# Kernel optimization log

Measured on AMD Instinct MI355X. Metric: run time of the kernel, lower is better.

Reference implementation:

```python
import jax, jax.numpy as jnp
import numpy as np

N = 10000
E = 320000
D_IN = 256
D_H = 256
D_OUT = 64
NEG_SLOPE = 0.2


def _segment_softmax(scores, seg, num_segments):
    # numerically stable softmax over variable-size neighborhoods
    m = jax.ops.segment_max(scores, seg, num_segments=num_segments)
    e = jnp.exp(scores - m[seg])
    s = jax.ops.segment_sum(e, seg, num_segments=num_segments)
    return e / s[seg]


def _gatv2_conv(x, src, dst, Wl, bl, Wr, br, att, bias):
    # PyG GATv2Conv, heads=1: lin_l on source, lin_r on target
    xl = x @ Wl + bl              # [N, C]
    xr = x @ Wr + br              # [N, C]
    xj = xl[src]                  # [E, C] source messages
    e = jax.nn.leaky_relu(xj + xr[dst], NEG_SLOPE)   # [E, C]
    score = e @ att               # [E]
    alpha = _segment_softmax(score, dst, N)          # [E]
    out = jax.ops.segment_sum(alpha[:, None] * xj, dst, num_segments=N)
    return out + bias


def setup_inputs() -> dict:
    key = jax.random.key(0)
    ks = jax.random.split(key, 16)
    s1 = 1.0 / np.sqrt(D_IN)
    s2 = 1.0 / np.sqrt(D_H)
    x = jax.random.normal(ks[0], (N, D_IN), dtype=jnp.float32)
    edge_index = jax.random.randint(ks[1], (2, E), 0, N, dtype=jnp.int64)
    return {
        "x": x,
        "W1l": jax.random.normal(ks[2], (D_IN, D_H), jnp.float32) * s1,
        "b1l": jnp.zeros((D_H,), jnp.float32),
        "W1r": jax.random.normal(ks[3], (D_IN, D_H), jnp.float32) * s1,
        "b1r": jnp.zeros((D_H,), jnp.float32),
        "att1": jax.random.normal(ks[4], (D_H,), jnp.float32) * s2,
        "bias1": jnp.zeros((D_H,), jnp.float32),
        "W2l": jax.random.normal(ks[5], (D_H, D_H), jnp.float32) * s2,
        "b2l": jnp.zeros((D_H,), jnp.float32),
        "W2r": jax.random.normal(ks[6], (D_H, D_H), jnp.float32) * s2,
        "b2r": jnp.zeros((D_H,), jnp.float32),
        "att2": jax.random.normal(ks[7], (D_H,), jnp.float32) * s2,
        "bias2": jnp.zeros((D_H,), jnp.float32),
        "Wout": jax.random.normal(ks[8], (D_H, D_OUT), jnp.float32) * s2,
        "bout": jnp.zeros((D_OUT,), jnp.float32),
        "edge_index": edge_index,
    }


def reference(x, W1l, b1l, W1r, b1r, att1, bias1,
              W2l, b2l, W2r, b2r, att2, bias2,
              Wout, bout, edge_index):
    # add self loops (PyG GATv2Conv default)
    loops = jnp.arange(N, dtype=edge_index.dtype)
    src = jnp.concatenate([edge_index[0], loops])
    dst = jnp.concatenate([edge_index[1], loops])

    h = _gatv2_conv(x, src, dst, W1l, b1l, W1r, b1r, att1, bias1)
    h = jax.nn.relu(h)            # norm=Identity, dropout inactive (eval)
    h = _gatv2_conv(h, src, dst, W2l, b2l, W2r, b2r, att2, bias2)
    h = jax.nn.relu(h)
    logits = h @ Wout + bout      # [N, D_OUT]
    return jax.nn.log_softmax(logits, axis=1)
```

## Files before the change

### kernel.cpp

```cpp
#include <hip/hip_runtime.h>
#include <hip/hip_bf16.h>
#include <math.h>

#define N_NODES 10000
#define N_EDGES 320000
#define TOT_E (N_EDGES + N_NODES)
#define D 256
#define DOUT 64
#define NEG_SLOPE 0.2f
#define MAXDEG 128

typedef __attribute__((ext_vector_type(8))) short bf16x8;
typedef __attribute__((ext_vector_type(4))) float f32x4;
typedef unsigned short ushort_t;

__device__ __forceinline__ unsigned short f2b_rne(float f) {
    unsigned int x = __float_as_uint(f);
    x += 0x7FFFu + ((x >> 16) & 1u);
    return (unsigned short)(x >> 16);
}
__device__ __forceinline__ float b2f(unsigned short h) {
    return __uint_as_float(((unsigned int)h) << 16);
}
__device__ __forceinline__ void bsplit(float v, unsigned short& hi, unsigned short& lo) {
    hi = f2b_rne(v);
    lo = f2b_rne(v - b2f(hi));
}

__device__ __forceinline__ void gload16(const ushort_t* g, ushort_t* l) {
    __builtin_amdgcn_global_load_lds(
        (const __attribute__((address_space(1))) void*)g,
        (__attribute__((address_space(3))) void*)l, 16, 0, 0);
}

__device__ __forceinline__ bool detect_f32(const void* x) {
    const ushort_t* xb = (const ushort_t*)x;
    int lane = threadIdx.x & 63;
    int bad = 0;
    #pragma unroll
    for (int i = 0; i < 4; ++i) {
        float v = b2f(xb[2 * (lane + 64 * i)]);
        bad += !(fabsf(v) < 1e4f) ? 1 : 0;
    }
    #pragma unroll
    for (int o = 32; o > 0; o >>= 1) bad += __shfl_down(bad, o);
    return __shfl(bad, 0) > 8;
}
__device__ __forceinline__ bool detect_i64(const int* e32) {
    int lane = threadIdx.x & 63;
    int nz = (e32[2 * lane + 1] != 0) ? 1 : 0;
    #pragma unroll
    for (int o = 32; o > 0; o >>= 1) nz += __shfl_down(nz, o);
    return __shfl(nz, 0) == 0;
}

__global__ __launch_bounds__(256) void prep_kernel(
        const void* x, ushort_t* xh, ushort_t* xlo,
        const void* W1l, const void* W1r, const void* W2l, const void* W2r, const void* Wo,
        const void* v0, const void* v1, const void* v2, const void* v3,
        const void* v4, const void* v5, const void* v6, const void* v7, const void* v8,
        ushort_t* wt, float* vecf, int* counts) {
    bool f32s = detect_f32(x);
    int bid = blockIdx.x;
    int t = threadIdx.x;
    if (bid < 2500) {
        int i = bid * 1024 + t * 4;
        float v[4];
        if (f32s) {
            float4 f = *(const float4*)((const float*)x + i);
            v[0] = f.x; v[1] = f.y; v[2] = f.z; v[3] = f.w;
        } else {
            union { uint2 q; ushort_t u[4]; } r;
            r.q = *(const uint2*)((const ushort_t*)x + i);
            #pragma unroll
            for (int j = 0; j < 4; ++j) v[j] = b2f(r.u[j]);
        }
        union { uint2 q; ushort_t u[4]; } H, L;
        #pragma unroll
        for (int j = 0; j < 4; ++j) bsplit(v[j], H.u[j], L.u[j]);
        *(uint2*)(xh + i) = H.q;
        *(uint2*)(xlo + i) = L.q;
    } else if (bid < 3588) {
        int b = bid - 2500;
        const void* srcs5[5] = {W1l, W1r, W2l, W2r, Wo};
        int wid, n, ncols;
        if (b < 1024) { wid = b >> 8; n = b & 255; ncols = 256; }
        else          { wid = 4;      n = b - 1024; ncols = 64; }
        ushort_t* dh;
        ushort_t* dl;
        if (wid < 4) { dh = wt + (size_t)wid * 2 * 65536; dl = dh + 65536; }
        else         { dh = wt + (size_t)8 * 65536;       dl = dh + 16384; }
        float v = f32s ? ((const float*)srcs5[wid])[(size_t)t * ncols + n]
                       : b2f(((const ushort_t*)srcs5[wid])[(size_t)t * ncols + n]);
        unsigned short hi, lo;
        bsplit(v, hi, lo);
        dh[(size_t)n * 256 + t] = hi;
        dl[(size_t)n * 256 + t] = lo;
    } else if (bid < 3597) {
        int b = bid - 3588;
        const void* ps[9] = {v0, v1, v2, v3, v4, v5, v6, v7, v8};
        int n = (b == 8) ? DOUT : 256;
        if (t < n) {
            float v = f32s ? ((const float*)ps[b])[t] : b2f(((const ushort_t*)ps[b])[t]);
            vecf[b * 256 + t] = v;
        }
    } else {
        int idx = (bid - 3597) * 256 + t;
        if (idx < N_NODES) counts[idx] = 0;
    }
}

__device__ __forceinline__ int eload(const int* ei, bool is64, int idx) {
    int v = is64 ? ei[2 * (size_t)idx] : ei[idx];
    return ((unsigned)v < (unsigned)N_NODES) ? v : 0;
}

__global__ __launch_bounds__(256) void scatter_kernel(const int* __restrict__ ei,
                                                      int* __restrict__ counts,
                                                      int* __restrict__ srcs_pad) {
    bool is64 = detect_i64(ei);
    int id = blockIdx.x * 256 + threadIdx.x;
    if (id >= TOT_E) return;
    int src, dst;
    if (id < N_EDGES) { src = eload(ei, is64, id); dst = eload(ei, is64, N_EDGES + id); }
    else              { src = dst = id - N_EDGES; }
    int slot = atomicAdd(&counts[dst], 1);
    if (slot < MAXDEG) srcs_pad[dst * MAXDEG + slot] = src;
}

__global__ __launch_bounds__(256, 3) void gemm_mfma_kernel(
        const ushort_t* __restrict__ Ahg, const ushort_t* __restrict__ Alg,
        const ushort_t* __restrict__ Wh0, const ushort_t* __restrict__ Wl0,
        const float* __restrict__ bias0, ushort_t* __restrict__ out0,
        const ushort_t* __restrict__ Wh1, const ushort_t* __restrict__ Wl1,
        const float* __restrict__ bias1, ushort_t* __restrict__ out1) {
    __shared__ __align__(16) ushort_t AhL[2][4096];
    __shared__ __align__(16) ushort_t AlL[2][4096];
    __shared__ __align__(16) ushort_t BhL[2][2048];
    __shared__ __align__(16) ushort_t BlL[2][2048];
    int tid = threadIdx.x;
    int lane = tid & 63, wave = tid >> 6;
    int lin = blockIdx.x + 8 * blockIdx.y;
    int v = (lin & 7) * 79 + (lin >> 3);
    int row0 = (v >> 3) * 128;
    int y = v & 7;
    const ushort_t* Wh; const ushort_t* Wl; const float* bias;
    ushort_t* outp;
    int col0;
    if (y < 4) { Wh = Wh0; Wl = Wl0; bias = bias0; col0 = y * 64; outp = out0; }
    else       { Wh = Wh1; Wl = Wl1; bias = bias1; col0 = (y - 4) * 64; outp = out1; }

    const ushort_t* gp[6];
    ushort_t* lp0[6];
    ushort_t* lp1[6];
    {
        int lane4 = lane >> 2;
        int qsl = (lane & 3) ^ (lane4 & 3);
        #pragma unroll
        for (int j = 0; j < 6; ++j) {
            int q = wave * 6 + j;
            if (q < 8) {
                gp[j] = Ahg + (size_t)(row0 + q * 16 + lane4) * 256 + qsl * 8;
                lp0[j] = &AhL[0][q * 512]; lp1[j] = &AhL[1][q * 512];
            } else if (q < 16) {
                int r = q - 8;
                gp[j] = Alg + (size_t)(row0 + r * 16 + lane4) * 256 + qsl * 8;
                lp0[j] = &AlL[0][r * 512]; lp1[j] = &AlL[1][r * 512];
            } else if (q < 20) {
                int r = q - 16;
                gp[j] = Wh + (size_t)(col0 + r * 16 + lane4) * 256 + qsl * 8;
                lp0[j] = &BhL[0][r * 512]; lp1[j] = &BhL[1][r * 512];
            } else {
                int r = q - 20;
                gp[j] = Wl + (size_t)(col0 + r * 16 + lane4) * 256 + qsl * 8;
                lp0[j] = &BlL[0][r * 512]; lp1[j] = &BlL[1][r * 512];
            }
        }
    }
    int wm = wave >> 1, wn = wave & 1;
    int l15 = lane & 15;
    int slot = (lane >> 4) ^ (lane & 3);

    f32x4 acc[4][2];
    #pragma unroll
    for (int mg = 0; mg < 4; ++mg)
        #pragma unroll
        for (int ng = 0; ng < 2; ++ng) acc[mg][ng] = (f32x4){0.f, 0.f, 0.f, 0.f};

    #pragma unroll
    for (int j = 0; j < 6; ++j) { gload16(gp[j], lp0[j]); gp[j] += 32; }
    __syncthreads();

    #pragma unroll
    for (int s = 0; s < 8; ++s) {
        const int cb = s & 1;
        if (s < 7) {
            #pragma unroll
            for (int j = 0; j < 6; ++j) {
                gload16(gp[j], cb ? lp0[j] : lp1[j]);
                gp[j] += 32;
            }
        }
        bf16x8 ah[4], al[4];
        #pragma unroll
        for (int mg = 0; mg < 4; ++mg) {
            int o = (wm * 64 + mg * 16 + l15) * 32 + slot * 8;
            ah[mg] = *(const bf16x8*)&AhL[cb][o];
            al[mg] = *(const bf16x8*)&AlL[cb][o];
        }
        #pragma unroll
        for (int ng = 0; ng < 2; ++ng) {
            int o = (wn * 32 + ng * 16 + l15) * 32 + slot * 8;
            bf16x8 b_h = *(const bf16x8*)&BhL[cb][o];
            bf16x8 b_l = *(const bf16x8*)&BlL[cb][o];
            #pragma unroll
            for (int mg = 0; mg < 4; ++mg) {
                acc[mg][ng] = __builtin_amdgcn_mfma_f32_16x16x32_bf16(ah[mg], b_l, acc[mg][ng], 0, 0, 0);
                acc[mg][ng] = __builtin_amdgcn_mfma_f32_16x16x32_bf16(al[mg], b_h, acc[mg][ng], 0, 0, 0);
                acc[mg][ng] = __builtin_amdgcn_mfma_f32_16x16x32_bf16(ah[mg], b_h, acc[mg][ng], 0, 0, 0);
            }
        }
        __syncthreads();
    }

    int quad = lane >> 4;
    #pragma unroll
    for (int ng = 0; ng < 2; ++ng) {
        int col = col0 + wn * 32 + ng * 16 + l15;
        float bv = bias[col];
        #pragma unroll
        for (int mg = 0; mg < 4; ++mg) {
            #pragma unroll
            for (int i = 0; i < 4; ++i) {
                int row = row0 + wm * 64 + mg * 16 + quad * 4 + i;
                if (row < N_NODES) {
                    float vv = acc[mg][ng][i] + bv;
                    outp[(size_t)row * D + col] = f2b_rne(vv);
                }
            }
        }
    }
}

__global__ __launch_bounds__(256) void quant_kernel(const ushort_t* __restrict__ xin,
                                                    unsigned char* __restrict__ xq,
                                                    float* __restrict__ xscale) {
    int lane = threadIdx.x & 63;
    int row = blockIdx.x * 4 + (threadIdx.x >> 6);
    if (row >= N_NODES) return;
    union { uint2 q; ushort_t u[4]; } r;
    r.q = *(const uint2*)(xin + (size_t)row * D + lane * 4);
    float v[4];
    float am = 0.f;
    #pragma unroll
    for (int j = 0; j < 4; ++j) {
        v[j] = b2f(r.u[j]);
        if (!isfinite(v[j])) v[j] = 0.f;
        am = fmaxf(am, fabsf(v[j]));
    }
    #pragma unroll
    for (int o = 32; o > 0; o >>= 1) am = fmaxf(am, __shfl_xor(am, o));
    float inv = (am > 0.f) ? 127.f / am : 0.f;
    unsigned int pk = 0;
    #pragma unroll
    for (int j = 0; j < 4; ++j) {
        int qv = (int)rintf(v[j] * inv);
        pk |= ((unsigned int)(qv & 255)) << (8 * j);
    }
    *(unsigned int*)(xq + (size_t)row * D + lane * 4) = pk;
    if (lane == 0) xscale[row] = (am > 0.f) ? am / 127.f : 0.f;
}

__global__ __launch_bounds__(256) void conv_kernel(const unsigned char* __restrict__ xq,
                                                   const float* __restrict__ xscale,
                                                   const ushort_t* __restrict__ xrb,
                                                   const float* __restrict__ att,
                                                   const float* __restrict__ bias,
                                                   const int* __restrict__ counts,
                                                   const int* __restrict__ srcs_pad,
                                                   ushort_t* __restrict__ hh,
                                                   ushort_t* __restrict__ hl) {
    __shared__ float fbuf[8][256];
    __shared__ float sred[8];
    int node = blockIdx.x;
    int t = threadIdx.x;
    int lane = t & 63;
    int hw = t >> 5;
    int seg = t & 31;
    int deg = counts[node];
    if (deg > MAXDEG) deg = MAXDEG;
    if (deg <= 0) {
        float o = fmaxf(bias[t], 0.f);
        unsigned short hi, lo; bsplit(o, hi, lo);
        hh[(size_t)node * D + t] = hi;
        hl[(size_t)node * D + t] = lo;
        return;
    }
    int s0 = srcs_pad[node * MAXDEG + lane];
    int s1 = srcs_pad[node * MAXDEG + 64 + lane];
    float xr8[8], att8[8];
    {
        union { uint4 q; ushort_t u[8]; } rr;
        rr.q = *(const uint4*)(xrb + (size_t)node * D + seg * 8);
        float4 a0 = *(const float4*)(att + seg * 8);
        float4 a1 = *(const float4*)(att + seg * 8 + 4);
        #pragma unroll
        for (int j = 0; j < 8; ++j) xr8[j] = b2f(rr.u[j]);
        att8[0] = a0.x; att8[1] = a0.y; att8[2] = a0.z; att8[3] = a0.w;
        att8[4] = a1.x; att8[5] = a1.y; att8[6] = a1.z; att8[7] = a1.w;
    }
    float acc8[8];
    #pragma unroll
    for (int j = 0; j < 8; ++j) acc8[j] = 0.f;
    float s = 0.f;

    for (int e0 = 0; e0 < deg; e0 += 32) {
        int dlim = deg - e0; if (dlim > 32) dlim = 32;
        int ni = (dlim > hw) ? ((dlim - hw + 7) >> 3) : 0;
        uint2 r[4];
        float se[4];
        #pragma unroll
        for (int i = 0; i < 4; ++i) {
            if (i < ni) {
                int e = e0 + hw + 8 * i;
                int src = __shfl((e < 64) ? s0 : s1, e & 63);
                r[i] = *(const uint2*)(xq + (size_t)src * D + seg * 8);
                se[i] = xscale[src];
            }
        }
        #pragma unroll
        for (int i = 0; i < 4; ++i) {
            if (i < ni) {
                float xf[8];
                #pragma unroll
                for (int j = 0; j < 8; ++j) {
                    unsigned int w32 = (j < 4) ? r[i].x : r[i].y;
                    int iv = ((int)(w32 << (24 - 8 * (j & 3)))) >> 24;
                    xf[j] = (float)iv * se[i];
                }
                float p = 0.f;
                #pragma unroll
                for (int j = 0; j < 8; ++j) {
                    float v = xf[j] + xr8[j];
                    v = fmaxf(v, NEG_SLOPE * v);
                    p = fmaf(v, att8[j], p);
                }
                #pragma unroll
                for (int o = 16; o > 0; o >>= 1) p += __shfl_xor(p, o, 32);
                p = __expf(fminf(fmaxf(p, -80.f), 80.f));
                s += p;
                #pragma unroll
                for (int j = 0; j < 8; ++j) acc8[j] = fmaf(p, xf[j], acc8[j]);
            }
        }
    }
    *(float4*)&fbuf[hw][seg * 8] = (float4){acc8[0], acc8[1], acc8[2], acc8[3]};
    *(float4*)&fbuf[hw][seg * 8 + 4] = (float4){acc8[4], acc8[5], acc8[6], acc8[7]};
    if (seg == 0) sred[hw] = s;
    __syncthreads();
    float tot = 0.f;
    #pragma unroll
    for (int k = 0; k < 8; ++k) tot += fbuf[k][t];
    float stot = sred[0];
    #pragma unroll
    for (int k = 1; k < 8; ++k) stot += sred[k];
    float o = tot / stot + bias[t];
    if (!isfinite(o)) o = 0.f;
    o = fmaxf(o, 0.f);
    unsigned short hi, lo; bsplit(o, hi, lo);
    hh[(size_t)node * D + t] = hi;
    hl[(size_t)node * D + t] = lo;
}

__global__ __launch_bounds__(256) void logits_kernel(
        const ushort_t* __restrict__ Ahg, const ushort_t* __restrict__ Alg,
        const ushort_t* __restrict__ Wh, const ushort_t* __restrict__ Wl,
        const float* __restrict__ bias, float* __restrict__ out) {
    __shared__ bf16x8 Ah[4][64];
    __shared__ bf16x8 Al[4][64];
    __shared__ bf16x8 Bh[4][64];
    __shared__ bf16x8 Bl[4][64];
    __shared__ float Cs[64][65];
    __shared__ float mxs[64], lss[64];
    int tid = threadIdx.x;
    int lane = tid & 63, wave = tid >> 6;
    int row0 = blockIdx.x * 64;
    int sm = tid >> 2, skq = tid & 3;
    int sl = skq * 16 + (sm & 15), sr = sm >> 4;

    f32x4 acc[4];
    #pragma unroll
    for (int c = 0; c < 4; ++c) acc[c] = (f32x4){0.f, 0.f, 0.f, 0.f};

    for (int k0 = 0; k0 < D; k0 += 32) {
        uint4 qah, qal;
        int grow = row0 + sm;
        if (grow < N_NODES) {
            size_t aoff = (size_t)grow * D + k0 + skq * 8;
            qah = *(const uint4*)(Ahg + aoff);
            qal = *(const uint4*)(Alg + aoff);
        } else {
            qah = (uint4){0, 0, 0, 0}; qal = (uint4){0, 0, 0, 0};
        }
        size_t boff = (size_t)sm * 256 + k0 + skq * 8;
        uint4 qbh = *(const uint4*)(Wh + boff);
        uint4 qbl = *(const uint4*)(Wl + boff);
        __syncthreads();
        *(uint4*)&Ah[sr][sl] = qah;
        *(uint4*)&Al[sr][sl] = qal;
        *(uint4*)&Bh[sr][sl] = qbh;
        *(uint4*)&Bl[sr][sl] = qbl;
        __syncthreads();
        bf16x8 a_h = Ah[wave][lane];
        bf16x8 a_l = Al[wave][lane];
        #pragma unroll
        for (int c = 0; c < 4; ++c) {
            bf16x8 b_h = Bh[c][lane];
            bf16x8 b_l = Bl[c][lane];
            acc[c] = __builtin_amdgcn_mfma_f32_16x16x32_bf16(a_h, b_l, acc[c], 0, 0, 0);
            acc[c] = __builtin_amdgcn_mfma_f32_16x16x32_bf16(a_l, b_h, acc[c], 0, 0, 0);
            acc[c] = __builtin_amdgcn_mfma_f32_16x16x32_bf16(a_h, b_h, acc[c], 0, 0, 0);
        }
    }
    int quad = lane >> 4;
    #pragma unroll
    for (int c = 0; c < 4; ++c) {
        int col = c * 16 + (lane & 15);
        float bv = bias[col];
        #pragma unroll
        for (int i = 0; i < 4; ++i) {
            int row = wave * 16 + quad * 4 + i;
            Cs[row][col] = acc[c][i] + bv;
        }
    }
    __syncthreads();
    if (tid < 64) {
        float mx = -INFINITY;
        for (int c2 = 0; c2 < 64; ++c2) {
            float v = Cs[tid][c2];
            if (!isfinite(v)) { v = -1e30f; Cs[tid][c2] = v; }
            mx = fmaxf(mx, v);
        }
        float ssum = 0.f;
        for (int c2 = 0; c2 < 64; ++c2) ssum += expf(Cs[tid][c2] - mx);
        mxs[tid] = mx;
        lss[tid] = logf(ssum);
    }
    __syncthreads();
    for (int idx = tid; idx < 64 * 64; idx += 256) {
        int r = idx >> 6, col = idx & 63;
        int grow = row0 + r;
        if (grow < N_NODES) out[(size_t)grow * DOUT + col] = Cs[r][col] - mxs[r] - lss[r];
    }
}

extern "C" void kernel_launch(void* const* d_in, const int* in_sizes, int n_in,
                              void* d_out, int out_size, void* d_ws, size_t ws_size,
                              hipStream_t stream) {
    const void* x    = d_in[0];
    const void* W1l  = d_in[1];
    const void* b1l  = d_in[2];
    const void* W1r  = d_in[3];
    const void* b1r  = d_in[4];
    const void* att1 = d_in[5];
    const void* bia1 = d_in[6];
    const void* W2l  = d_in[7];
    const void* b2l  = d_in[8];
    const void* W2r  = d_in[9];
    const void* b2r  = d_in[10];
    const void* att2 = d_in[11];
    const void* bia2 = d_in[12];
    const void* Wout = d_in[13];
    const void* bout = d_in[14];
    const int*  ei   = (const int*)d_in[15];

    int* counts   = (int*)d_ws;
    int* srcs_pad = counts + N_NODES;
    ushort_t* wt = (ushort_t*)(srcs_pad + (size_t)N_NODES * MAXDEG);
    ushort_t* W1lH = wt;                ushort_t* W1lL = W1lH + 65536;
    ushort_t* W1rH = W1lL + 65536;      ushort_t* W1rL = W1rH + 65536;
    ushort_t* W2lH = W1rL + 65536;      ushort_t* W2lL = W2lH + 65536;
    ushort_t* W2rH = W2lL + 65536;      ushort_t* W2rL = W2rH + 65536;
    ushort_t* WoH  = W2rL + 65536;      ushort_t* WoL  = WoH + 16384;
    float* vecf = (float*)(WoL + 16384);
    ushort_t* xh  = (ushort_t*)(vecf + 9 * 256);
    ushort_t* xlo = xh + (size_t)N_NODES * D;
    ushort_t* xlb = xlo + (size_t)N_NODES * D;
    ushort_t* xrb = xlb + (size_t)N_NODES * D;
    unsigned char* xq = (unsigned char*)(xrb + (size_t)N_NODES * D);
    float* xscale = (float*)(xq + (size_t)N_NODES * D);
    ushort_t* hh = xh;
    ushort_t* hl = xlo;

    float* b1lf = vecf + 0 * 256;
    float* b1rf = vecf + 1 * 256;
    float* att1f = vecf + 2 * 256;
    float* bia1f = vecf + 3 * 256;
    float* b2lf = vecf + 4 * 256;
    float* b2rf = vecf + 5 * 256;
    float* att2f = vecf + 6 * 256;
    float* bia2f = vecf + 7 * 256;
    float* boutf = vecf + 8 * 256;

    prep_kernel<<<3637, 256, 0, stream>>>(x, xh, xlo,
                                          W1l, W1r, W2l, W2r, Wout,
                                          b1l, b1r, att1, bia1, b2l, b2r, att2, bia2, bout,
                                          wt, vecf, counts);
    scatter_kernel<<<(TOT_E + 255) / 256, 256, 0, stream>>>(ei, counts, srcs_pad);

    gemm_mfma_kernel<<<dim3(8, 79), 256, 0, stream>>>(
        xh, xlo, W1lH, W1lL, b1lf, xlb, W1rH, W1rL, b1rf, xrb);
    quant_kernel<<<(N_NODES + 3) / 4, 256, 0, stream>>>(xlb, xq, xscale);
    conv_kernel<<<N_NODES, 256, 0, stream>>>(xq, xscale, xrb, att1f, bia1f,
                                             counts, srcs_pad, hh, hl);
    gemm_mfma_kernel<<<dim3(8, 79), 256, 0, stream>>>(
        hh, hl, W2lH, W2lL, b2lf, xlb, W2rH, W2rL, b2rf, xrb);
    quant_kernel<<<(N_NODES + 3) / 4, 256, 0, stream>>>(xlb, xq, xscale);
    conv_kernel<<<N_NODES, 256, 0, stream>>>(xq, xscale, xrb, att2f, bia2f,
                                             counts, srcs_pad, hh, hl);
    logits_kernel<<<(N_NODES + 63) / 64, 256, 0, stream>>>(hh, hl, WoH, WoL, boutf, (float*)d_out);
}
```

Baseline: 237.5 us.

## Fold edge scatter into first GEMM launch and gather bf16 messages directly

The edge scatter, which builds the padded neighbor lists, now runs as extra blocks appended to the first GEMM grid, removing a separate launch and letting it overlap with GEMM tiles. The int8 quantization kernels are removed, and the conv kernel gathers bf16 source rows directly. This drops two launches and the quantize pass, but doubles the bytes read per gathered neighbor (16 instead of 8 per segment). It also removes an approximation, since int8 messages reduced accuracy.

```diff
diff --git a/kernel.cpp b/kernel.cpp
--- a/kernel.cpp
+++ b/kernel.cpp
@@ -115,31 +115,34 @@
     return ((unsigned)v < (unsigned)N_NODES) ? v : 0;
 }
 
-__global__ __launch_bounds__(256) void scatter_kernel(const int* __restrict__ ei,
-                                                      int* __restrict__ counts,
-                                                      int* __restrict__ srcs_pad) {
-    bool is64 = detect_i64(ei);
-    int id = blockIdx.x * 256 + threadIdx.x;
-    if (id >= TOT_E) return;
-    int src, dst;
-    if (id < N_EDGES) { src = eload(ei, is64, id); dst = eload(ei, is64, N_EDGES + id); }
-    else              { src = dst = id - N_EDGES; }
-    int slot = atomicAdd(&counts[dst], 1);
-    if (slot < MAXDEG) srcs_pad[dst * MAXDEG + slot] = src;
-}
-
 __global__ __launch_bounds__(256, 3) void gemm_mfma_kernel(
         const ushort_t* __restrict__ Ahg, const ushort_t* __restrict__ Alg,
         const ushort_t* __restrict__ Wh0, const ushort_t* __restrict__ Wl0,
         const float* __restrict__ bias0, ushort_t* __restrict__ out0,
         const ushort_t* __restrict__ Wh1, const ushort_t* __restrict__ Wl1,
-        const float* __restrict__ bias1, ushort_t* __restrict__ out1) {
+        const float* __restrict__ bias1, ushort_t* __restrict__ out1,
+        const int* __restrict__ ei, int* __restrict__ counts,
+        int* __restrict__ srcs_pad) {
     __shared__ __align__(16) ushort_t AhL[2][4096];
     __shared__ __align__(16) ushort_t AlL[2][4096];
     __shared__ __align__(16) ushort_t BhL[2][2048];
     __shared__ __align__(16) ushort_t BlL[2][2048];
     int tid = threadIdx.x;
     int lane = tid & 63, wave = tid >> 6;
+
+    if (blockIdx.y >= 79) {
+        bool is64 = detect_i64(ei);
+        int id = ((blockIdx.y - 79) * 8 + blockIdx.x) * 256 + tid;
+        if (id < TOT_E) {
+            int src, dst;
+            if (id < N_EDGES) { src = eload(ei, is64, id); dst = eload(ei, is64, N_EDGES + id); }
+            else              { src = dst = id - N_EDGES; }
+            int slot = atomicAdd(&counts[dst], 1);
+            if (slot < MAXDEG) srcs_pad[dst * MAXDEG + slot] = src;
+        }
+        return;
+    }
+
     int lin = blockIdx.x + 8 * blockIdx.y;
     int v = (lin & 7) * 79 + (lin >> 3);
     int row0 = (v >> 3) * 128;
@@ -242,37 +245,7 @@
     }
 }
 
-__global__ __launch_bounds__(256) void quant_kernel(const ushort_t* __restrict__ xin,
-                                                    unsigned char* __restrict__ xq,
-                                                    float* __restrict__ xscale) {
-    int lane = threadIdx.x & 63;
-    int row = blockIdx.x * 4 + (threadIdx.x >> 6);
-    if (row >= N_NODES) return;
-    union { uint2 q; ushort_t u[4]; } r;
-    r.q = *(const uint2*)(xin + (size_t)row * D + lane * 4);
-    float v[4];
-    float am = 0.f;
-    #pragma unroll
-    for (int j = 0; j < 4; ++j) {
-        v[j] = b2f(r.u[j]);
-        if (!isfinite(v[j])) v[j] = 0.f;
-        am = fmaxf(am, fabsf(v[j]));
-    }
-    #pragma unroll
-    for (int o = 32; o > 0; o >>= 1) am = fmaxf(am, __shfl_xor(am, o));
-    float inv = (am > 0.f) ? 127.f / am : 0.f;
-    unsigned int pk = 0;
-    #pragma unroll
-    for (int j = 0; j < 4; ++j) {
-        int qv = (int)rintf(v[j] * inv);
-        pk |= ((unsigned int)(qv & 255)) << (8 * j);
-    }
-    *(unsigned int*)(xq + (size_t)row * D + lane * 4) = pk;
-    if (lane == 0) xscale[row] = (am > 0.f) ? am / 127.f : 0.f;
-}
-
-__global__ __launch_bounds__(256) void conv_kernel(const unsigned char* __restrict__ xq,
-                                                   const float* __restrict__ xscale,
+__global__ __launch_bounds__(256) void conv_kernel(const ushort_t* __restrict__ xl,
                                                    const ushort_t* __restrict__ xrb,
                                                    const float* __restrict__ att,
                                                    const float* __restrict__ bias,
@@ -317,15 +290,13 @@
     for (int e0 = 0; e0 < deg; e0 += 32) {
         int dlim = deg - e0; if (dlim > 32) dlim = 32;
         int ni = (dlim > hw) ? ((dlim - hw + 7) >> 3) : 0;
-        uint2 r[4];
-        float se[4];
+        union { uint4 q; ushort_t u[8]; } r[4];
         #pragma unroll
         for (int i = 0; i < 4; ++i) {
             if (i < ni) {
                 int e = e0 + hw + 8 * i;
                 int src = __shfl((e < 64) ? s0 : s1, e & 63);
-                r[i] = *(const uint2*)(xq + (size_t)src * D + seg * 8);
-                se[i] = xscale[src];
+                r[i].q = *(const uint4*)(xl + (size_t)src * D + seg * 8);
             }
         }
         #pragma unroll
@@ -333,11 +304,7 @@
             if (i < ni) {
                 float xf[8];
                 #pragma unroll
-                for (int j = 0; j < 8; ++j) {
-                    unsigned int w32 = (j < 4) ? r[i].x : r[i].y;
-                    int iv = ((int)(w32 << (24 - 8 * (j & 3)))) >> 24;
-                    xf[j] = (float)iv * se[i];
-                }
+                for (int j = 0; j < 8; ++j) xf[j] = b2f(r[i].u[j]);
                 float p = 0.f;
                 #pragma unroll
                 for (int j = 0; j < 8; ++j) {
@@ -487,8 +454,6 @@
     ushort_t* xlo = xh + (size_t)N_NODES * D;
     ushort_t* xlb = xlo + (size_t)N_NODES * D;
     ushort_t* xrb = xlb + (size_t)N_NODES * D;
-    unsigned char* xq = (unsigned char*)(xrb + (size_t)N_NODES * D);
-    float* xscale = (float*)(xq + (size_t)N_NODES * D);
     ushort_t* hh = xh;
     ushort_t* hl = xlo;
 
@@ -506,17 +471,16 @@
                                           W1l, W1r, W2l, W2r, Wout,
                                           b1l, b1r, att1, bia1, b2l, b2r, att2, bia2, bout,
                                           wt, vecf, counts);
-    scatter_kernel<<<(TOT_E + 255) / 256, 256, 0, stream>>>(ei, counts, srcs_pad);
-
-    gemm_mfma_kernel<<<dim3(8, 79), 256, 0, stream>>>(
-        xh, xlo, W1lH, W1lL, b1lf, xlb, W1rH, W1rL, b1rf, xrb);
-    quant_kernel<<<(N_NODES + 3) / 4, 256, 0, stream>>>(xlb, xq, xscale);
-    conv_kernel<<<N_NODES, 256, 0, stream>>>(xq, xscale, xrb, att1f, bia1f,
+
+    gemm_mfma_kernel<<<dim3(8, 79 + 162), 256, 0, stream>>>(
+        xh, xlo, W1lH, W1lL, b1lf, xlb, W1rH, W1rL, b1rf, xrb,
+        ei, counts, srcs_pad);
+    conv_kernel<<<N_NODES, 256, 0, stream>>>(xlb, xrb, att1f, bia1f,
                                              counts, srcs_pad, hh, hl);
     gemm_mfma_kernel<<<dim3(8, 79), 256, 0, stream>>>(
-        hh, hl, W2lH, W2lL, b2lf, xlb, W2rH, W2rL, b2rf, xrb);
-    quant_kernel<<<(N_NODES + 3) / 4, 256, 0, stream>>>(xlb, xq, xscale);
-    conv_kernel<<<N_NODES, 256, 0, stream>>>(xq, xscale, xrb, att2f, bia2f,
+        hh, hl, W2lH, W2lL, b2lf, xlb, W2rH, W2rL, b2rf, xrb,
+        nullptr, nullptr, nullptr);
+    conv_kernel<<<N_NODES, 256, 0, stream>>>(xlb, xrb, att2f, bia2f,
                                              counts, srcs_pad, hh, hl);
     logits_kernel<<<(N_NODES + 63) / 64, 256, 0, stream>>>(hh, hl, WoH, WoL, boutf, (float*)d_out);
 }
```

Result: faster. 218.7 us (-7.9%).
